# Performance work log

Measured on AMD Instinct MI355X. Metric: run time of the kernel, lower is better.

Reference implementation:

```python
import jax, jax.numpy as jnp
import numpy as np

RADIUS = 0.1
MAX_NEIGHBORS = 64


def setup_inputs() -> dict:
    key0 = jax.random.key(0)
    k1, k2 = jax.random.split(key0)
    query = jax.random.uniform(k1, (4, 2048, 3), dtype=jnp.float32)
    key = jax.random.uniform(k2, (4, 8192, 3), dtype=jnp.float32)
    return {"query": query, "key": key}


def reference(query, key):
    # PointNet++-style ball query: for each query point, the indices of the
    # first MAX_NEIGHBORS key points (in key order) with squared distance
    # < RADIUS^2; remaining slots are padded with the first found neighbor
    # index (0 if no neighbor exists, matching zero-initialized CUDA output).
    B, N1, _ = query.shape
    N2 = key.shape[1]
    K = MAX_NEIGHBORS

    # [B, N1, N2] squared pairwise distances
    d2 = jnp.sum((query[:, :, None, :] - key[:, None, :, :]) ** 2, axis=-1)
    within = d2 < jnp.float32(RADIUS) ** 2  # [B, N1, N2] bool

    # slot each valid neighbor lands in (in key-index order)
    pos = jnp.cumsum(within.astype(jnp.int32), axis=-1) - 1  # [B, N1, N2]
    take = within & (pos < K)
    slot = jnp.where(take, pos, K)  # invalid entries routed to dummy slot K

    n2_idx = jnp.broadcast_to(jnp.arange(N2, dtype=jnp.int32), (B, N1, N2))
    b_idx = jnp.arange(B)[:, None, None]
    n1_idx = jnp.arange(N1)[None, :, None]

    out = jnp.full((B, N1, K + 1), -1, dtype=jnp.int32)
    # slots < K are unique per (b, n1); duplicates only at dummy slot K
    out = out.at[b_idx, n1_idx, slot].set(n2_idx)
    out = out[..., :K]  # drop dummy slot

    # pad empty slots with index of first in-radius neighbor (0 if none)
    first = jnp.argmax(within, axis=-1).astype(jnp.int32)  # [B, N1]
    out = jnp.where(out < 0, first[..., None], out)
    return out
```

## Files before the change

kernel.cpp:

```cpp
#include <hip/hip_runtime.h>


constexpr int   K    = 64;
constexpr float R2   = 0.01f;
constexpr int   B    = 4;
constexpr int   N1   = 2048;
constexpr int   N2   = 8192;
constexpr int   GC   = 5;
constexpr int   NCELL = GC * GC * GC;
constexpr float INVCELL = 5.0f;

constexpr size_t SORTED_BYTES = (size_t)B * N2 * 16;
constexpr size_t WS_NEEDED    = SORTED_BYTES + (size_t)(B * (NCELL + 1)) * 4;

__device__ __forceinline__ int cell_of(float v) {
    int c = (int)(v * INVCELL);
    return c < 0 ? 0 : (c > GC - 1 ? GC - 1 : c);
}

__global__ __launch_bounds__(1024) void build_kernel(
    const float* __restrict__ key,
    float4* __restrict__ sorted,
    int* __restrict__ cell_start)
{
    __shared__ int hist[NCELL];
    __shared__ int sbuf[128];
    __shared__ int start[NCELL + 1];

    const int b = blockIdx.x;
    const int t = threadIdx.x;
    constexpr int PER = N2 / 1024;

    if (t < NCELL) hist[t] = 0;
    __syncthreads();

    const float* kb = key + (size_t)b * N2 * 3;
    int mycell[PER];
    #pragma unroll
    for (int r = 0; r < PER; ++r) {
        const int i = r * 1024 + t;
        const float x = kb[i * 3 + 0];
        const float y = kb[i * 3 + 1];
        const float z = kb[i * 3 + 2];
        const int cell = (cell_of(x) * GC + cell_of(y)) * GC + cell_of(z);
        mycell[r] = cell;
        atomicAdd(&hist[cell], 1);
    }
    __syncthreads();

    if (t < 128) sbuf[t] = (t < NCELL) ? hist[t] : 0;
    __syncthreads();
    for (int off = 1; off < 128; off <<= 1) {
        int v = 0;
        if (t < 128 && t >= off) v = sbuf[t - off];
        __syncthreads();
        if (t < 128) sbuf[t] += v;
        __syncthreads();
    }
    if (t < NCELL) start[t + 1] = sbuf[t];
    if (t == 0)    start[0] = 0;
    __syncthreads();
    if (t < NCELL + 1) cell_start[b * (NCELL + 1) + t] = start[t];
    if (t < NCELL)     hist[t] = start[t];
    __syncthreads();

    float4* sb = sorted + (size_t)b * N2;
    #pragma unroll
    for (int r = 0; r < PER; ++r) {
        const int i = r * 1024 + t;
        const int cell = mycell[r];
        const int pos = atomicAdd(&hist[cell], 1);
        float4 v;
        v.x = kb[i * 3 + 0];
        v.y = kb[i * 3 + 1];
        v.z = kb[i * 3 + 2];
        v.w = __int_as_float(i);
        sb[pos] = v;
    }
}

__global__ __launch_bounds__(256) void ballquery_grid_kernel(
    const float* __restrict__ query,
    const float4* __restrict__ sorted,
    const int* __restrict__ cell_start,
    int* __restrict__ out)
{
    __shared__ unsigned int bm[4 * 256];

    const int lane = threadIdx.x & 63;
    const int wv   = threadIdx.x >> 6;
    const int q    = blockIdx.x * 4 + wv;
    const int b    = q >> 11;

    const float qx = query[q * 3 + 0];
    const float qy = query[q * 3 + 1];
    const float qz = query[q * 3 + 2];

    const float ux = qx * INVCELL, uy = qy * INVCELL, uz = qz * INVCELL;
    const int cx = cell_of(qx), cy = cell_of(qy), cz = cell_of(qz);
    const int nx = (ux - cx < 0.5f) ? cx - 1 : cx + 1;
    const int ny = (uy - cy < 0.5f) ? cy - 1 : cy + 1;
    const int nz = (uz - cz < 0.5f) ? cz - 1 : cz + 1;
    const int xlo = max(0, min(cx, nx)), xhi = min(GC - 1, max(cx, nx));
    const int ylo = max(0, min(cy, ny)), yhi = min(GC - 1, max(cy, ny));
    const int zlo = max(0, min(cz, nz)), zhi = min(GC - 1, max(cz, nz));

    unsigned int* wbm = bm + wv * 256;
    uint4 zz; zz.x = zz.y = zz.z = zz.w = 0u;
    ((uint4*)wbm)[lane] = zz;
    __threadfence_block();

    const int*    cs = cell_start + b * (NCELL + 1);
    const float4* sb = sorted + (size_t)b * N2;

    for (int xx = xlo; xx <= xhi; ++xx) {
        for (int yy = ylo; yy <= yhi; ++yy) {
            const int colz = (xx * GC + yy) * GC;
            const int s = cs[colz + zlo];
            const int e = cs[colz + zhi + 1];
            for (int t0 = s; t0 < e; t0 += 64) {
                const int i = t0 + lane;
                const float4 kv = sb[min(i, e - 1)];
                const float dx = kv.x - qx;
                const float dy = kv.y - qy;
                const float dz = kv.z - qz;
                const bool within = (i < e) && (dx * dx + dy * dy + dz * dz < R2);
                if (within) {
                    const int id = __float_as_int(kv.w);
                    atomicOr(&wbm[id >> 5], 1u << (id & 31));
                }
            }
        }
    }
    __threadfence_block();

    const uint4 w = ((const uint4*)wbm)[lane];
    const int c = __popc(w.x) + __popc(w.y) + __popc(w.z) + __popc(w.w);

    int x = c;
    #pragma unroll
    for (int off = 1; off < 64; off <<= 1) {
        int y = __shfl_up(x, off);
        if (lane >= off) x += y;
    }
    const int base = x - c;
    const int cnt  = __shfl(x, 63);

    int fs;
    if      (w.x) fs = __builtin_ctz(w.x);
    else if (w.y) fs = 32 + __builtin_ctz(w.y);
    else if (w.z) fs = 64 + __builtin_ctz(w.z);
    else if (w.w) fs = 96 + __builtin_ctz(w.w);
    else          fs = 0;
    int myfirst = c ? (lane << 7) + fs : 0x7fffffff;
    #pragma unroll
    for (int off = 32; off; off >>= 1)
        myfirst = min(myfirst, __shfl_xor(myfirst, off));
    const int firstIdx = (cnt == 0) ? 0 : myfirst;

    int* op = out + q * K;
    int slot = base;
    unsigned int wr[4] = {w.x, w.y, w.z, w.w};
    #pragma unroll
    for (int r = 0; r < 4; ++r) {
        unsigned int m = wr[r];
        const int bb = (lane << 7) + (r << 5);
        while (m) {
            const int bp = __builtin_ctz(m);
            m &= m - 1;
            if (slot < K) op[slot] = bb + bp;
            ++slot;
        }
    }

    const int kpad = cnt < K ? cnt : K;
    const int s2 = kpad + lane;
    if (s2 < K) op[s2] = firstIdx;
}

__global__ __launch_bounds__(256) void ballquery_bruteforce_kernel(
    const float* __restrict__ query, const float* __restrict__ key,
    int* __restrict__ out)
{
    const int lane = threadIdx.x & 63;
    const int q = blockIdx.x * 4 + (threadIdx.x >> 6);
    const int b = q >> 11;
    const float qx = query[q * 3], qy = query[q * 3 + 1], qz = query[q * 3 + 2];
    const float* kb = key + (size_t)b * N2 * 3;
    int* op = out + (size_t)q * K;
    int count = 0, first = 0;
    bool have_first = false;
    const unsigned long long lane_mask_lt = (lane == 0) ? 0ull : (~0ull >> (64 - lane));
    for (int c = 0; c < N2 / 64; ++c) {
        if (count >= K) break;
        const int j = (c << 6) + lane;
        const float* kp = kb + j * 3;
        const float dx = kp[0] - qx, dy = kp[1] - qy, dz = kp[2] - qz;
        const bool within = dx * dx + dy * dy + dz * dz < R2;
        const unsigned long long mask = __ballot(within);
        if (mask) {
            if (!have_first) { first = (c << 6) + __builtin_ctzll(mask); have_first = true; }
            if (within) {
                const int slot = count + __popcll(mask & lane_mask_lt);
                if (slot < K) op[slot] = j;
            }
            count += __popcll(mask);
        }
    }
    const int cnt = count < K ? count : K;
    if (cnt + lane < K) op[cnt + lane] = first;
}

extern "C" void kernel_launch(void* const* d_in, const int* in_sizes, int n_in,
                              void* d_out, int out_size, void* d_ws, size_t ws_size,
                              hipStream_t stream) {
    const float* query = (const float*)d_in[0];
    const float* key   = (const float*)d_in[1];
    int* out = (int*)d_out;

    if (ws_size < WS_NEEDED) {
        ballquery_bruteforce_kernel<<<(B * N1) / 4, 256, 0, stream>>>(query, key, out);
        return;
    }

    float4* sorted     = (float4*)d_ws;
    int*    cell_start = (int*)((char*)d_ws + SORTED_BYTES);

    build_kernel<<<B, 1024, 0, stream>>>(key, sorted, cell_start);
    ballquery_grid_kernel<<<(B * N1) / 4, 256, 0, stream>>>(query, sorted, cell_start, out);
}
```

Baseline: 74.40 us.

## Fuse grid build and query into one kernel with per-block shared-memory sorted keys

```diff
diff --git a/kernel.cpp b/kernel.cpp
--- a/kernel.cpp
+++ b/kernel.cpp
@@ -9,27 +9,31 @@
 constexpr int   GC   = 5;
 constexpr int   NCELL = GC * GC * GC;
 constexpr float INVCELL = 5.0f;
-
-constexpr size_t SORTED_BYTES = (size_t)B * N2 * 16;
-constexpr size_t WS_NEEDED    = SORTED_BYTES + (size_t)(B * (NCELL + 1)) * 4;
+constexpr int   BLOCKS = 256;
+constexpr int   QPW    = 8;
+constexpr int   PER    = N2 / 256;
 
 __device__ __forceinline__ int cell_of(float v) {
     int c = (int)(v * INVCELL);
     return c < 0 ? 0 : (c > GC - 1 ? GC - 1 : c);
 }
 
-__global__ __launch_bounds__(1024) void build_kernel(
+__global__ __launch_bounds__(256) void ballquery_fused_kernel(
+    const float* __restrict__ query,
     const float* __restrict__ key,
-    float4* __restrict__ sorted,
-    int* __restrict__ cell_start)
+    int* __restrict__ out)
 {
-    __shared__ int hist[NCELL];
-    __shared__ int sbuf[128];
-    __shared__ int start[NCELL + 1];
+    __shared__ float4 skey[N2];
+    __shared__ int    hist[NCELL];
+    __shared__ int    sbuf[128];
+    __shared__ int    start[NCELL + 1];
+    __shared__ unsigned int bm[4 * 256];
 
-    const int b = blockIdx.x;
-    const int t = threadIdx.x;
-    constexpr int PER = N2 / 1024;
+    const int blk  = blockIdx.x;
+    const int b    = blk >> 6;
+    const int t    = threadIdx.x;
+    const int lane = t & 63;
+    const int wv   = t >> 6;
 
     if (t < NCELL) hist[t] = 0;
     __syncthreads();
@@ -38,7 +42,7 @@
     int mycell[PER];
     #pragma unroll
     for (int r = 0; r < PER; ++r) {
-        const int i = r * 1024 + t;
+        const int i = r * 256 + t;
         const float x = kb[i * 3 + 0];
         const float y = kb[i * 3 + 1];
         const float z = kb[i * 3 + 2];
@@ -60,155 +64,110 @@
     if (t < NCELL) start[t + 1] = sbuf[t];
     if (t == 0)    start[0] = 0;
     __syncthreads();
-    if (t < NCELL + 1) cell_start[b * (NCELL + 1) + t] = start[t];
-    if (t < NCELL)     hist[t] = start[t];
+    if (t < NCELL) hist[t] = start[t];
     __syncthreads();
 
-    float4* sb = sorted + (size_t)b * N2;
     #pragma unroll
     for (int r = 0; r < PER; ++r) {
-        const int i = r * 1024 + t;
-        const int cell = mycell[r];
-        const int pos = atomicAdd(&hist[cell], 1);
+        const int i = r * 256 + t;
+        const int pos = atomicAdd(&hist[mycell[r]], 1);
         float4 v;
         v.x = kb[i * 3 + 0];
         v.y = kb[i * 3 + 1];
         v.z = kb[i * 3 + 2];
         v.w = __int_as_float(i);
-        sb[pos] = v;
+        skey[pos] = v;
     }
-}
-
-__global__ __launch_bounds__(256) void ballquery_grid_kernel(
-    const float* __restrict__ query,
-    const float4* __restrict__ sorted,
-    const int* __restrict__ cell_start,
-    int* __restrict__ out)
-{
-    __shared__ unsigned int bm[4 * 256];
-
-    const int lane = threadIdx.x & 63;
-    const int wv   = threadIdx.x >> 6;
-    const int q    = blockIdx.x * 4 + wv;
-    const int b    = q >> 11;
-
-    const float qx = query[q * 3 + 0];
-    const float qy = query[q * 3 + 1];
-    const float qz = query[q * 3 + 2];
-
-    const float ux = qx * INVCELL, uy = qy * INVCELL, uz = qz * INVCELL;
-    const int cx = cell_of(qx), cy = cell_of(qy), cz = cell_of(qz);
-    const int nx = (ux - cx < 0.5f) ? cx - 1 : cx + 1;
-    const int ny = (uy - cy < 0.5f) ? cy - 1 : cy + 1;
-    const int nz = (uz - cz < 0.5f) ? cz - 1 : cz + 1;
-    const int xlo = max(0, min(cx, nx)), xhi = min(GC - 1, max(cx, nx));
-    const int ylo = max(0, min(cy, ny)), yhi = min(GC - 1, max(cy, ny));
-    const int zlo = max(0, min(cz, nz)), zhi = min(GC - 1, max(cz, nz));
+    __syncthreads();
 
     unsigned int* wbm = bm + wv * 256;
-    uint4 zz; zz.x = zz.y = zz.z = zz.w = 0u;
-    ((uint4*)wbm)[lane] = zz;
-    __threadfence_block();
+    const int qbase = blk * (4 * QPW) + wv * QPW;
 
-    const int*    cs = cell_start + b * (NCELL + 1);
-    const float4* sb = sorted + (size_t)b * N2;
+    for (int qi = 0; qi < QPW; ++qi) {
+        const int q = qbase + qi;
 
-    for (int xx = xlo; xx <= xhi; ++xx) {
-        for (int yy = ylo; yy <= yhi; ++yy) {
-            const int colz = (xx * GC + yy) * GC;
-            const int s = cs[colz + zlo];
-            const int e = cs[colz + zhi + 1];
-            for (int t0 = s; t0 < e; t0 += 64) {
-                const int i = t0 + lane;
-                const float4 kv = sb[min(i, e - 1)];
-                const float dx = kv.x - qx;
-                const float dy = kv.y - qy;
-                const float dz = kv.z - qz;
-                const bool within = (i < e) && (dx * dx + dy * dy + dz * dz < R2);
-                if (within) {
-                    const int id = __float_as_int(kv.w);
-                    atomicOr(&wbm[id >> 5], 1u << (id & 31));
+        const float qx = query[q * 3 + 0];
+        const float qy = query[q * 3 + 1];
+        const float qz = query[q * 3 + 2];
+
+        const float ux = qx * INVCELL, uy = qy * INVCELL, uz = qz * INVCELL;
+        const int cx = cell_of(qx), cy = cell_of(qy), cz = cell_of(qz);
+        const int nx = (ux - cx < 0.5f) ? cx - 1 : cx + 1;
+        const int ny = (uy - cy < 0.5f) ? cy - 1 : cy + 1;
+        const int nz = (uz - cz < 0.5f) ? cz - 1 : cz + 1;
+        const int xlo = max(0, min(cx, nx)), xhi = min(GC - 1, max(cx, nx));
+        const int ylo = max(0, min(cy, ny)), yhi = min(GC - 1, max(cy, ny));
+        const int zlo = max(0, min(cz, nz)), zhi = min(GC - 1, max(cz, nz));
+
+        uint4 zz; zz.x = zz.y = zz.z = zz.w = 0u;
+        ((uint4*)wbm)[lane] = zz;
+        __threadfence_block();
+
+        for (int xx = xlo; xx <= xhi; ++xx) {
+            for (int yy = ylo; yy <= yhi; ++yy) {
+                const int colz = (xx * GC + yy) * GC;
+                const int s = start[colz + zlo];
+                const int e = start[colz + zhi + 1];
+                for (int t0 = s; t0 < e; t0 += 64) {
+                    const int i = t0 + lane;
+                    const float4 kv = skey[min(i, e - 1)];
+                    const float dx = kv.x - qx;
+                    const float dy = kv.y - qy;
+                    const float dz = kv.z - qz;
+                    const bool within = (i < e) &&
+                        (dx * dx + dy * dy + dz * dz < R2);
+                    if (within) {
+                        const int id = __float_as_int(kv.w);
+                        atomicOr(&wbm[id >> 5], 1u << (id & 31));
+                    }
                 }
             }
         }
+        __threadfence_block();
+
+        const uint4 w = ((const uint4*)wbm)[lane];
+        const int c = __popc(w.x) + __popc(w.y) + __popc(w.z) + __popc(w.w);
+
+        int x = c;
+        #pragma unroll
+        for (int off = 1; off < 64; off <<= 1) {
+            int y = __shfl_up(x, off);
+            if (lane >= off) x += y;
+        }
+        const int base = x - c;
+        const int cnt  = __shfl(x, 63);
+
+        int fs;
+        if      (w.x) fs = __builtin_ctz(w.x);
+        else if (w.y) fs = 32 + __builtin_ctz(w.y);
+        else if (w.z) fs = 64 + __builtin_ctz(w.z);
+        else if (w.w) fs = 96 + __builtin_ctz(w.w);
+        else          fs = 0;
+        int myfirst = c ? (lane << 7) + fs : 0x7fffffff;
+        #pragma unroll
+        for (int off = 32; off; off >>= 1)
+            myfirst = min(myfirst, __shfl_xor(myfirst, off));
+        const int firstIdx = (cnt == 0) ? 0 : myfirst;
+
+        int* op = out + q * K;
+        int slot = base;
+        unsigned int wr[4] = {w.x, w.y, w.z, w.w};
+        #pragma unroll
+        for (int r = 0; r < 4; ++r) {
+            unsigned int m = wr[r];
+            const int bb = (lane << 7) + (r << 5);
+            while (m) {
+                const int bp = __builtin_ctz(m);
+                m &= m - 1;
+                if (slot < K) op[slot] = bb + bp;
+                ++slot;
+            }
+        }
+
+        const int kpad = cnt < K ? cnt : K;
+        const int s2 = kpad + lane;
+        if (s2 < K) op[s2] = firstIdx;
     }
-    __threadfence_block();
-
-    const uint4 w = ((const uint4*)wbm)[lane];
-    const int c = __popc(w.x) + __popc(w.y) + __popc(w.z) + __popc(w.w);
-
-    int x = c;
-    #pragma unroll
-    for (int off = 1; off < 64; off <<= 1) {
-        int y = __shfl_up(x, off);
-        if (lane >= off) x += y;
-    }
-    const int base = x - c;
-    const int cnt  = __shfl(x, 63);
-
-    int fs;
-    if      (w.x) fs = __builtin_ctz(w.x);
-    else if (w.y) fs = 32 + __builtin_ctz(w.y);
-    else if (w.z) fs = 64 + __builtin_ctz(w.z);
-    else if (w.w) fs = 96 + __builtin_ctz(w.w);
-    else          fs = 0;
-    int myfirst = c ? (lane << 7) + fs : 0x7fffffff;
-    #pragma unroll
-    for (int off = 32; off; off >>= 1)
-        myfirst = min(myfirst, __shfl_xor(myfirst, off));
-    const int firstIdx = (cnt == 0) ? 0 : myfirst;
-
-    int* op = out + q * K;
-    int slot = base;
-    unsigned int wr[4] = {w.x, w.y, w.z, w.w};
-    #pragma unroll
-    for (int r = 0; r < 4; ++r) {
-        unsigned int m = wr[r];
-        const int bb = (lane << 7) + (r << 5);
-        while (m) {
-            const int bp = __builtin_ctz(m);
-            m &= m - 1;
-            if (slot < K) op[slot] = bb + bp;
-            ++slot;
-        }
-    }
-
-    const int kpad = cnt < K ? cnt : K;
-    const int s2 = kpad + lane;
-    if (s2 < K) op[s2] = firstIdx;
-}
-
-__global__ __launch_bounds__(256) void ballquery_bruteforce_kernel(
-    const float* __restrict__ query, const float* __restrict__ key,
-    int* __restrict__ out)
-{
-    const int lane = threadIdx.x & 63;
-    const int q = blockIdx.x * 4 + (threadIdx.x >> 6);
-    const int b = q >> 11;
-    const float qx = query[q * 3], qy = query[q * 3 + 1], qz = query[q * 3 + 2];
-    const float* kb = key + (size_t)b * N2 * 3;
-    int* op = out + (size_t)q * K;
-    int count = 0, first = 0;
-    bool have_first = false;
-    const unsigned long long lane_mask_lt = (lane == 0) ? 0ull : (~0ull >> (64 - lane));
-    for (int c = 0; c < N2 / 64; ++c) {
-        if (count >= K) break;
-        const int j = (c << 6) + lane;
-        const float* kp = kb + j * 3;
-        const float dx = kp[0] - qx, dy = kp[1] - qy, dz = kp[2] - qz;
-        const bool within = dx * dx + dy * dy + dz * dz < R2;
-        const unsigned long long mask = __ballot(within);
-        if (mask) {
-            if (!have_first) { first = (c << 6) + __builtin_ctzll(mask); have_first = true; }
-            if (within) {
-                const int slot = count + __popcll(mask & lane_mask_lt);
-                if (slot < K) op[slot] = j;
-            }
-            count += __popcll(mask);
-        }
-    }
-    const int cnt = count < K ? count : K;
-    if (cnt + lane < K) op[cnt + lane] = first;
 }
 
 extern "C" void kernel_launch(void* const* d_in, const int* in_sizes, int n_in,
@@ -218,14 +177,5 @@
     const float* key   = (const float*)d_in[1];
     int* out = (int*)d_out;
 
-    if (ws_size < WS_NEEDED) {
-        ballquery_bruteforce_kernel<<<(B * N1) / 4, 256, 0, stream>>>(query, key, out);
-        return;
-    }
-
-    float4* sorted     = (float4*)d_ws;
-    int*    cell_start = (int*)((char*)d_ws + SORTED_BYTES);
-
-    build_kernel<<<B, 1024, 0, stream>>>(key, sorted, cell_start);
-    ballquery_grid_kernel<<<(B * N1) / 4, 256, 0, stream>>>(query, sorted, cell_start, out);
+    ballquery_fused_kernel<<<BLOCKS, 256, 0, stream>>>(query, key, out);
 }
```

Result: slower. 93.69 us (+25.9%).
